# Kernel tuning notes

Hardware: AMD Instinct MI355X
Metric: run time of the kernel (lower is better)

## Reference

```python
import jax, jax.numpy as jnp
import numpy as np

B, S = 4, 512
D_IN, D_H = 1600, 1600
HEADS = 50
PH = D_H // HEADS  # 32, per-head size
N_REL = 100


def setup_inputs() -> dict:
    key = jax.random.key(0)
    ks = jax.random.split(key, 14)
    w = lambda k, shape: (jax.random.normal(k, shape, jnp.float32) * 0.02)
    return {
        "hidden": jax.random.normal(ks[0], (B, S, D_IN), jnp.float32),
        "Wq": w(ks[1], (D_IN, D_H)), "bq": jnp.zeros((D_H,), jnp.float32),
        "Wk": w(ks[2], (D_IN, D_H)), "bk": jnp.zeros((D_H,), jnp.float32),
        "Wv": w(ks[3], (D_IN, D_H)), "bv": jnp.zeros((D_H,), jnp.float32),
        "Wo": w(ks[4], (D_H, D_H)), "bo": jnp.zeros((D_H,), jnp.float32),
        "rel_k_emb": w(ks[5], (N_REL, PH)),
        "rel_v_emb": w(ks[6], (N_REL, PH)),
        "W1": w(ks[7], (D_H, D_H)), "b1": jnp.zeros((D_H,), jnp.float32),
        "W2": w(ks[8], (D_H, D_H)), "b2": jnp.zeros((D_H,), jnp.float32),
        "relationship_matrix": jax.random.randint(ks[9], (B, S, S), 0, N_REL),
    }


def reference(hidden, Wq, bq, Wk, bk, Wv, bv, Wo, bo,
              rel_k_emb, rel_v_emb, W1, b1, W2, b2, relationship_matrix):
    b, s, _ = hidden.shape

    def split_heads(x):  # [b,s,D_H] -> [b,h,s,ph]
        return x.reshape(b, s, HEADS, PH).transpose(0, 2, 1, 3)

    q = split_heads(hidden @ Wq + bq)
    k = split_heads(hidden @ Wk + bk)
    v = split_heads(hidden @ Wv + bv)

    # relation-aware bias: gather per-(query,key) relation embeddings
    rel_k = rel_k_emb[relationship_matrix]  # [b,s,s,ph]
    rel_v = rel_v_emb[relationship_matrix]  # [b,s,s,ph]

    scores = jnp.einsum('bhqd,bhkd->bhqk', q, k) \
           + jnp.einsum('bhqd,bqkd->bhqk', q, rel_k)
    probs = jax.nn.softmax(scores / np.float32(np.sqrt(PH)), axis=-1)

    ctx = jnp.einsum('bhqk,bhkd->bhqd', probs, v) \
        + jnp.einsum('bhqk,bqkd->bhqd', probs, rel_v)
    ctx = ctx.transpose(0, 2, 1, 3).reshape(b, s, D_H)
    attn_out = ctx @ Wo + bo

    # position-wise FFN (hidden -> hidden -> hidden), exact gelu
    h = jax.nn.gelu(attn_out @ W1 + b1, approximate=False)
    return h @ W2 + b2
```

## Files before the change

### kernel.cpp

```cpp
#include <hip/hip_runtime.h>
#include <math.h>

#define B_   4
#define S_   512
#define DH   1600
#define NH   50
#define PH   32
#define NREL 100
#define MROWS (B_ * S_)

typedef _Float16 f16x8 __attribute__((ext_vector_type(8)));
typedef float  floatx4 __attribute__((ext_vector_type(4)));

__device__ __forceinline__ float gelu_f(float x) {
    return 0.5f * x * (1.0f + erff(x * 0.70710678118654752f));
}

__device__ __forceinline__ unsigned short f2h_u(float f) {
    _Float16 h = (_Float16)f;
    return __builtin_bit_cast(unsigned short, h);
}

typedef const __attribute__((address_space(1))) unsigned int guint;
typedef __attribute__((address_space(3))) unsigned int luint;
__device__ __forceinline__ void gl_lds16(const unsigned short* g, unsigned short* l)
{
    __builtin_amdgcn_global_load_lds((guint*)g, (luint*)l, 16, 0, 0);
}

__global__ __launch_bounds__(256)
void fcast_k(const float* __restrict__ in, unsigned short* __restrict__ out, int n4)
{
    int i = blockIdx.x * 256 + threadIdx.x;
    if (i < n4) {
        float4 v = *(const float4*)&in[i * 4];
        ushort4 o = { f2h_u(v.x), f2h_u(v.y), f2h_u(v.z), f2h_u(v.w) };
        *(ushort4*)&out[i * 4] = o;
    }
}

__global__ __launch_bounds__(256)
void wcast_k(const float* __restrict__ W0, const float* __restrict__ W1,
             const float* __restrict__ W2, const float* __restrict__ W3,
             const float* __restrict__ W4, const float* __restrict__ W5,
             unsigned short* __restrict__ T)
{
    const int z = blockIdx.z;
    const float* W = (z==0)?W0:(z==1)?W1:(z==2)?W2:(z==3)?W3:(z==4)?W4:W5;
    unsigned short* out = T + (size_t)z * DH * DH;

    __shared__ float tile[32][33];
    const int t = threadIdx.x;
    const int n0 = blockIdx.x * 32, k0 = blockIdx.y * 32;
    const int r = t >> 3, c4 = (t & 7) * 4;

    float4 v = *(const float4*)&W[(size_t)(k0 + r) * DH + n0 + c4];
    tile[r][c4 + 0] = v.x; tile[r][c4 + 1] = v.y;
    tile[r][c4 + 2] = v.z; tile[r][c4 + 3] = v.w;
    __syncthreads();

    ushort4 o = { f2h_u(tile[c4 + 0][r]), f2h_u(tile[c4 + 1][r]),
                  f2h_u(tile[c4 + 2][r]), f2h_u(tile[c4 + 3][r]) };
    *(ushort4*)&out[(size_t)(n0 + r) * DH + k0 + c4] = o;
}

#define BM 128
#define BN 64
#define BK 64

template<bool GELU, bool WF32, bool WF16>
__global__ __launch_bounds__(256)
void gemm_f16_k(const unsigned short* __restrict__ Ab,
                const unsigned short* __restrict__ Bt0,
                const unsigned short* __restrict__ Bt1,
                const unsigned short* __restrict__ Bt2,
                const float* __restrict__ bi0, const float* __restrict__ bi1,
                const float* __restrict__ bi2,
                float* __restrict__ Cf0, float* __restrict__ Cf1, float* __restrict__ Cf2,
                unsigned short* __restrict__ Ch0, unsigned short* __restrict__ Ch1,
                unsigned short* __restrict__ Ch2)
{
    const int z = blockIdx.z;
    const unsigned short* Bt = (z==0)?Bt0:(z==1)?Bt1:Bt2;
    const float* bi = (z==0)?bi0:(z==1)?bi1:bi2;
    float* Cf = (z==0)?Cf0:(z==1)?Cf1:Cf2;
    unsigned short* Ch = (z==0)?Ch0:(z==1)?Ch1:Ch2;

    __shared__ __align__(16) unsigned short As[BM * BK];
    __shared__ __align__(16) unsigned short Bs[BN * BK];

    const int tid = threadIdx.x;
    const int lane = tid & 63, w = tid >> 6;
    const int bm = blockIdx.y * BM, bn = blockIdx.x * BN;
    const int wm = (w >> 1) * 64, wn = (w & 1) * 32;

    const int lr8 = lane >> 3;
    const int sgrp = ((lane & 7) ^ lr8) * 8;

    const int fl_m = lane & 15, quad = lane >> 4;
    const int rs = fl_m & 7;
    const int g0 = (quad ^ rs) * 8;

    floatx4 acc[4][2] = {};

    for (int k0 = 0; k0 < DH; k0 += BK) {
        __syncthreads();
        #pragma unroll
        for (int c = 0; c < 4; c++) {
            int rowb = (c * 4 + w) * 8;
            gl_lds16(&Ab[(size_t)(bm + rowb + lr8) * DH + k0 + sgrp],
                     &As[(c * 4 + w) * 512]);
        }
        #pragma unroll
        for (int c = 0; c < 2; c++) {
            int rowb = (c * 4 + w) * 8;
            gl_lds16(&Bt[(size_t)(bn + rowb + lr8) * DH + k0 + sgrp],
                     &Bs[(c * 4 + w) * 512]);
        }
        __syncthreads();

        f16x8 af[2][4], bf[2][2];
        #pragma unroll
        for (int kk = 0; kk < 2; kk++) {
            const int gg = g0 ^ (kk * 32);
            #pragma unroll
            for (int mt = 0; mt < 4; mt++)
                af[kk][mt] = *(const f16x8*)&As[(wm + mt * 16 + fl_m) * 64 + gg];
            #pragma unroll
            for (int nt = 0; nt < 2; nt++)
                bf[kk][nt] = *(const f16x8*)&Bs[(wn + nt * 16 + fl_m) * 64 + gg];
        }

        #pragma unroll
        for (int kk = 0; kk < 2; kk++)
            #pragma unroll
            for (int mt = 0; mt < 4; mt++)
                #pragma unroll
                for (int nt = 0; nt < 2; nt++)
                    acc[mt][nt] = __builtin_amdgcn_mfma_f32_16x16x32_f16(
                        af[kk][mt], bf[kk][nt], acc[mt][nt], 0, 0, 0);
    }

    const int row_q = (lane >> 4) * 4;
    #pragma unroll
    for (int mt = 0; mt < 4; mt++) {
        #pragma unroll
        for (int nt = 0; nt < 2; nt++) {
            const int col = bn + wn + nt * 16 + fl_m;
            const float bias = bi[col];
            #pragma unroll
            for (int r = 0; r < 4; r++) {
                const int row = bm + wm + mt * 16 + row_q + r;
                float v = acc[mt][nt][r] + bias;
                if (GELU) v = gelu_f(v);
                if (WF32) Cf[(size_t)row * DH + col] = v;
                if (WF16) Ch[(size_t)row * DH + col] = f2h_u(v);
            }
        }
    }
}

__global__ __launch_bounds__(256, 1)
void attn_k(const unsigned short* __restrict__ Qg,
            const unsigned short* __restrict__ Kg,
            const unsigned short* __restrict__ Vg,
            const float* __restrict__ relk, const float* __restrict__ relv,
            const int* __restrict__ RM, unsigned short* __restrict__ CTX)
{
    __shared__ union {
        unsigned short Kb[512 * 40];
        unsigned short VT[32 * 520];
        float          qf[64 * 36];
    } big;
    __shared__ unsigned char rmb[64 * 516];
    __shared__ float qrel[64 * 101];
    __shared__ float wsum[64 * 101];
    __shared__ float relb[NREL * 36];
    __shared__ unsigned short Pb[4][2][16 * 40];

    const int tid = threadIdx.x;
    const int w = tid >> 6, lane = tid & 63;
    const int cl = lane & 15, quad = lane >> 4;
    const int b = blockIdx.z, h = blockIdx.y, q0 = blockIdx.x * 64;
    const float scale = 0.17677669529663689f;

    for (int i = tid; i < 64 * 101; i += 256) wsum[i] = 0.f;
    {
        int row = tid >> 2, g = tid & 3;
        uint4 qv = *(const uint4*)&Qg[(size_t)(b * S_ + q0 + row) * DH + h * PH + g * 8];
        f16x8 qh = __builtin_bit_cast(f16x8, qv);
        #pragma unroll
        for (int j = 0; j < 8; j++) big.qf[row * 36 + g * 8 + j] = (float)qh[j];
    }
    for (int i = tid; i < NREL * 8; i += 256) {
        int r = i >> 3, dg = i & 7;
        *(float4*)&relb[r * 36 + dg * 4] = *(const float4*)&relk[r * PH + dg * 4];
    }
    #pragma unroll
    for (int it = 0; it < 32; it++) {
        int idx = it * 256 + tid;
        int key4 = idx & 127, ql = idx >> 7;
        int4 rv = *(const int4*)&RM[(size_t)(b * S_ + q0 + ql) * S_ + key4 * 4];
        uchar4 o = { (unsigned char)rv.x, (unsigned char)rv.y,
                     (unsigned char)rv.z, (unsigned char)rv.w };
        *(uchar4*)&rmb[ql * 516 + key4 * 4] = o;
    }
    __syncthreads();

    {
        const int q = tid >> 2, rsub = tid & 3;
        float qv[PH];
        #pragma unroll
        for (int d = 0; d < PH; d++) qv[d] = big.qf[q * 36 + d];
        for (int i = 0; i < 25; i++) {
            int r = rsub * 25 + i;
            float s = 0.f;
            #pragma unroll
            for (int d = 0; d < PH; d++) s += qv[d] * relb[r * 36 + d];
            qrel[q * 101 + r] = s;
        }
    }
    __syncthreads();

    #pragma unroll
    for (int it = 0; it < 8; it++) {
        int idx = it * 256 + tid;
        int key = idx >> 2, g = idx & 3;
        uint4 kv = *(const uint4*)&Kg[(size_t)(b * S_ + key) * DH + h * PH + g * 8];
        *(uint4*)&big.Kb[key * 40 + g * 8] = kv;
    }
    for (int i = tid; i < NREL * 8; i += 256) {
        int r = i >> 3, dg = i & 7;
        *(float4*)&relb[r * 36 + dg * 4] = *(const float4*)&relv[r * PH + dg * 4];
    }
    __syncthreads();

    floatx4 acc[32];
    {
        f16x8 qa = __builtin_bit_cast(f16x8, *(const uint4*)
            &Qg[(size_t)(b * S_ + q0 + w * 16 + cl) * DH + h * PH + quad * 8]);
        #pragma unroll
        for (int t = 0; t < 32; t++) {
            f16x8 kf = *(const f16x8*)&big.Kb[(t * 16 + cl) * 40 + quad * 8];
            acc[t] = __builtin_amdgcn_mfma_f32_16x16x32_f16(qa, kf, (floatx4){}, 0, 0, 0);
        }
        #pragma unroll
        for (int t = 0; t < 32; t++) {
            #pragma unroll
            for (int r = 0; r < 4; r++) {
                int ql = w * 16 + quad * 4 + r;
                int rm = rmb[ql * 516 + t * 16 + cl];
                acc[t][r] = (acc[t][r] + qrel[ql * 101 + rm]) * scale;
            }
        }
        float mx[4] = {-1e30f, -1e30f, -1e30f, -1e30f};
        #pragma unroll
        for (int t = 0; t < 32; t++)
            #pragma unroll
            for (int r = 0; r < 4; r++) mx[r] = fmaxf(mx[r], acc[t][r]);
        #pragma unroll
        for (int r = 0; r < 4; r++) {
            #pragma unroll
            for (int off = 1; off < 16; off <<= 1)
                mx[r] = fmaxf(mx[r], __shfl_xor(mx[r], off));
        }
        float sm[4] = {};
        #pragma unroll
        for (int t = 0; t < 32; t++)
            #pragma unroll
            for (int r = 0; r < 4; r++) {
                float e = __expf(acc[t][r] - mx[r]);
                acc[t][r] = e; sm[r] += e;
            }
        #pragma unroll
        for (int r = 0; r < 4; r++) {
            #pragma unroll
            for (int off = 1; off < 16; off <<= 1)
                sm[r] += __shfl_xor(sm[r], off);
            sm[r] = 1.0f / sm[r];
        }
        #pragma unroll
        for (int t = 0; t < 32; t++)
            #pragma unroll
            for (int r = 0; r < 4; r++) acc[t][r] *= sm[r];
        #pragma unroll
        for (int t = 0; t < 32; t++) {
            #pragma unroll
            for (int r = 0; r < 4; r++) {
                int ql = w * 16 + quad * 4 + r;
                int rm = rmb[ql * 516 + t * 16 + cl];
                atomicAdd(&wsum[ql * 101 + rm], acc[t][r]);
            }
        }
    }
    __syncthreads();

    #pragma unroll
    for (int it = 0; it < 8; it++) {
        int idx = it * 256 + tid;
        int key = idx >> 2, part = idx & 3;
        uint4 vv = *(const uint4*)&Vg[(size_t)(b * S_ + key) * DH + h * PH + part * 8];
        f16x8 vh = __builtin_bit_cast(f16x8, vv);
        #pragma unroll
        for (int j = 0; j < 8; j++)
            big.VT[(part * 8 + j) * 520 + key] = f2h_u((float)vh[j]) , (void)0;
    }
    __syncthreads();

    {
        floatx4 ctx[2] = {};
        #pragma unroll
        for (int c = 0; c < 16; c++) {
            #pragma unroll
            for (int tt = 0; tt < 2; tt++) {
                #pragma unroll
                for (int r = 0; r < 4; r++)
                    Pb[w][c & 1][(quad * 4 + r) * 40 + tt * 16 + cl] =
                        f2h_u(acc[c * 2 + tt][r]);
            }
            f16x8 pa = *(const f16x8*)&Pb[w][c & 1][cl * 40 + quad * 8];
            #pragma unroll
            for (int nt = 0; nt < 2; nt++) {
                f16x8 vf = *(const f16x8*)&big.VT[(nt * 16 + cl) * 520 + c * 32 + quad * 8];
                ctx[nt] = __builtin_amdgcn_mfma_f32_16x16x32_f16(pa, vf, ctx[nt], 0, 0, 0);
            }
        }
        for (int r = 0; r < NREL; r++) {
            float rv0 = relb[r * 36 + cl];
            float rv1 = relb[r * 36 + 16 + cl];
            #pragma unroll
            for (int rr = 0; rr < 4; rr++) {
                float ws = wsum[(w * 16 + quad * 4 + rr) * 101 + r];
                ctx[0][rr] += ws * rv0;
                ctx[1][rr] += ws * rv1;
            }
        }
        #pragma unroll
        for (int nt = 0; nt < 2; nt++) {
            #pragma unroll
            for (int rr = 0; rr < 4; rr++) {
                int row = b * S_ + q0 + w * 16 + quad * 4 + rr;
                int col = h * PH + nt * 16 + cl;
                CTX[(size_t)row * DH + col] = f2h_u(ctx[nt][rr]);
            }
        }
    }
}

extern "C" void kernel_launch(void* const* d_in, const int* in_sizes, int n_in,
                              void* d_out, int out_size, void* d_ws, size_t ws_size,
                              hipStream_t stream)
{
    const float* hidden = (const float*)d_in[0];
    const float* Wq = (const float*)d_in[1];  const float* bq = (const float*)d_in[2];
    const float* Wk = (const float*)d_in[3];  const float* bk = (const float*)d_in[4];
    const float* Wv = (const float*)d_in[5];  const float* bv = (const float*)d_in[6];
    const float* Wo = (const float*)d_in[7];  const float* bo = (const float*)d_in[8];
    const float* relk = (const float*)d_in[9];
    const float* relv = (const float*)d_in[10];
    const float* W1 = (const float*)d_in[11]; const float* b1 = (const float*)d_in[12];
    const float* W2 = (const float*)d_in[13]; const float* b2 = (const float*)d_in[14];
    const int*   RM = (const int*)d_in[15];
    float* out = (float*)d_out;

    const size_t SZ = (size_t)MROWS * DH;
    const size_t SZB = SZ * 2;

    char* ws = (char*)d_ws;
    unsigned short* hb   = (unsigned short*)(ws);
    unsigned short* qf   = (unsigned short*)(ws + SZB);
    unsigned short* kf   = (unsigned short*)(ws + 2*SZB);
    unsigned short* vf   = (unsigned short*)(ws + 3*SZB);
    unsigned short* ctxf = (unsigned short*)(ws + 4*SZB);
    unsigned short* aof  = (unsigned short*)(ws + 5*SZB);
    unsigned short* hff  = (unsigned short*)(ws + 6*SZB);
    unsigned short* Wt   = (unsigned short*)(ws + 7*SZB);
    const size_t WSZ = (size_t)DH * DH;
    unsigned short *Wtq = Wt,         *Wtk = Wt + WSZ,   *Wtv = Wt + 2*WSZ,
                   *Wto = Wt + 3*WSZ, *Wt1 = Wt + 4*WSZ, *Wt2 = Wt + 5*WSZ;

    fcast_k<<<dim3((SZ/4 + 255)/256), 256, 0, stream>>>(hidden, hb, (int)(SZ/4));
    wcast_k<<<dim3(DH/32, DH/32, 6), 256, 0, stream>>>(Wq, Wk, Wv, Wo, W1, W2, Wt);

    gemm_f16_k<false, false, true><<<dim3(DH/BN, MROWS/BM, 3), 256, 0, stream>>>(
        hb, Wtq, Wtk, Wtv, bq, bk, bv,
        nullptr, nullptr, nullptr, qf, kf, vf);

    attn_k<<<dim3(S_/64, NH, B_), 256, 0, stream>>>(qf, kf, vf, relk, relv, RM, ctxf);

    gemm_f16_k<false, false, true><<<dim3(DH/BN, MROWS/BM, 1), 256, 0, stream>>>(
        ctxf, Wto, Wto, Wto, bo, bo, bo,
        nullptr, nullptr, nullptr, aof, aof, aof);

    gemm_f16_k<true, false, true><<<dim3(DH/BN, MROWS/BM, 1), 256, 0, stream>>>(
        aof, Wt1, Wt1, Wt1, b1, b1, b1,
        nullptr, nullptr, nullptr, hff, hff, hff);

    gemm_f16_k<false, true, false><<<dim3(DH/BN, MROWS/BM, 1), 256, 0, stream>>>(
        hff, Wt2, Wt2, Wt2, b2, b2, b2,
        out, out, out, nullptr, nullptr, nullptr);
}
```

Before: 723.6 us.

## Fuse QKV GEMMs sharing A tile and add XCD-aware block swizzle

Adds a dedicated QKV kernel that loads each activation tile into LDS once and multiplies it against the Q, K and V weight tiles, so the activation matrix is not read three times. Also remaps block indices so consecutive tiles land on the same XCD, for better L2 locality across all GEMMs. The fused kernel holds three times the accumulators and more LDS, which raises register pressure and may lower occupancy. The grid is also one third the size, giving fewer blocks to spread across CUs.

```diff
diff --git a/kernel.cpp b/kernel.cpp
--- a/kernel.cpp
+++ b/kernel.cpp
@@ -26,6 +26,15 @@
 __device__ __forceinline__ void gl_lds16(const unsigned short* g, unsigned short* l)
 {
     __builtin_amdgcn_global_load_lds((guint*)g, (luint*)l, 16, 0, 0);
+}
+
+__device__ __forceinline__ void xcd_swizzle(int& bx, int& by)
+{
+    const int nx = gridDim.x, nwg = nx * gridDim.y;
+    const int lin = blockIdx.y * nx + blockIdx.x;
+    const int cpx = nwg >> 3;
+    const int swz = (lin & 7) * cpx + (lin >> 3);
+    bx = swz % nx; by = swz / nx;
 }
 
 __global__ __launch_bounds__(256)
@@ -91,7 +100,8 @@
 
     const int tid = threadIdx.x;
     const int lane = tid & 63, w = tid >> 6;
-    const int bm = blockIdx.y * BM, bn = blockIdx.x * BN;
+    int bx, by; xcd_swizzle(bx, by);
+    const int bm = by * BM, bn = bx * BN;
     const int wm = (w >> 1) * 64, wn = (w & 1) * 32;
 
     const int lr8 = lane >> 3;
@@ -155,6 +165,96 @@
                 if (GELU) v = gelu_f(v);
                 if (WF32) Cf[(size_t)row * DH + col] = v;
                 if (WF16) Ch[(size_t)row * DH + col] = f2h_u(v);
+            }
+        }
+    }
+}
+
+__global__ __launch_bounds__(256)
+void gemm_qkv3_k(const unsigned short* __restrict__ Ab,
+                 const unsigned short* __restrict__ Bq,
+                 const unsigned short* __restrict__ Bk,
+                 const unsigned short* __restrict__ Bv,
+                 const float* __restrict__ bq, const float* __restrict__ bk,
+                 const float* __restrict__ bv,
+                 unsigned short* __restrict__ Cq, unsigned short* __restrict__ Ck,
+                 unsigned short* __restrict__ Cv)
+{
+    __shared__ __align__(16) unsigned short As[BM * BK];
+    __shared__ __align__(16) unsigned short Bs[3][BN * BK];
+
+    const int tid = threadIdx.x;
+    const int lane = tid & 63, w = tid >> 6;
+    int bx, by; xcd_swizzle(bx, by);
+    const int bm = by * BM, bn = bx * BN;
+    const int wm = (w >> 1) * 64, wn = (w & 1) * 32;
+
+    const int lr8 = lane >> 3;
+    const int sgrp = ((lane & 7) ^ lr8) * 8;
+
+    const int fl_m = lane & 15, quad = lane >> 4;
+    const int rs = fl_m & 7;
+    const int g0 = (quad ^ rs) * 8;
+
+    floatx4 acc[3][4][2] = {};
+
+    for (int k0 = 0; k0 < DH; k0 += BK) {
+        __syncthreads();
+        #pragma unroll
+        for (int c = 0; c < 4; c++) {
+            int rowb = (c * 4 + w) * 8;
+            gl_lds16(&Ab[(size_t)(bm + rowb + lr8) * DH + k0 + sgrp],
+                     &As[(c * 4 + w) * 512]);
+        }
+        #pragma unroll
+        for (int c = 0; c < 2; c++) {
+            int rowb = (c * 4 + w) * 8;
+            const size_t src = (size_t)(bn + rowb + lr8) * DH + k0 + sgrp;
+            gl_lds16(&Bq[src], &Bs[0][(c * 4 + w) * 512]);
+            gl_lds16(&Bk[src], &Bs[1][(c * 4 + w) * 512]);
+            gl_lds16(&Bv[src], &Bs[2][(c * 4 + w) * 512]);
+        }
+        __syncthreads();
+
+        #pragma unroll
+        for (int kk = 0; kk < 2; kk++) {
+            const int gg = g0 ^ (kk * 32);
+            f16x8 af[4];
+            #pragma unroll
+            for (int mt = 0; mt < 4; mt++)
+                af[mt] = *(const f16x8*)&As[(wm + mt * 16 + fl_m) * 64 + gg];
+            #pragma unroll
+            for (int z = 0; z < 3; z++) {
+                f16x8 bf[2];
+                #pragma unroll
+                for (int nt = 0; nt < 2; nt++)
+                    bf[nt] = *(const f16x8*)&Bs[z][(wn + nt * 16 + fl_m) * 64 + gg];
+                #pragma unroll
+                for (int mt = 0; mt < 4; mt++)
+                    #pragma unroll
+                    for (int nt = 0; nt < 2; nt++)
+                        acc[z][mt][nt] = __builtin_amdgcn_mfma_f32_16x16x32_f16(
+                            af[mt], bf[nt], acc[z][mt][nt], 0, 0, 0);
+            }
+        }
+    }
+
+    const int row_q = (lane >> 4) * 4;
+    #pragma unroll
+    for (int z = 0; z < 3; z++) {
+        const float* bi = (z==0)?bq:(z==1)?bk:bv;
+        unsigned short* Ch = (z==0)?Cq:(z==1)?Ck:Cv;
+        #pragma unroll
+        for (int mt = 0; mt < 4; mt++) {
+            #pragma unroll
+            for (int nt = 0; nt < 2; nt++) {
+                const int col = bn + wn + nt * 16 + fl_m;
+                const float bias = bi[col];
+                #pragma unroll
+                for (int r = 0; r < 4; r++) {
+                    const int row = bm + wm + mt * 16 + row_q + r;
+                    Ch[(size_t)row * DH + col] = f2h_u(acc[z][mt][nt][r] + bias);
+                }
             }
         }
     }
@@ -382,9 +482,8 @@
     fcast_k<<<dim3((SZ/4 + 255)/256), 256, 0, stream>>>(hidden, hb, (int)(SZ/4));
     wcast_k<<<dim3(DH/32, DH/32, 6), 256, 0, stream>>>(Wq, Wk, Wv, Wo, W1, W2, Wt);
 
-    gemm_f16_k<false, false, true><<<dim3(DH/BN, MROWS/BM, 3), 256, 0, stream>>>(
-        hb, Wtq, Wtk, Wtv, bq, bk, bv,
-        nullptr, nullptr, nullptr, qf, kf, vf);
+    gemm_qkv3_k<<<dim3(DH/BN, MROWS/BM), 256, 0, stream>>>(
+        hb, Wtq, Wtk, Wtv, bq, bk, bv, qf, kf, vf);
 
     attn_k<<<dim3(S_/64, NH, B_), 256, 0, stream>>>(qf, kf, vf, relk, relv, RM, ctxf);
 
```

Result: no change. 717.0 us (-0.9%).
